# Kernel tuning notes

Measured on AMD Instinct MI355X. Metric: run time of the kernel, lower is better.

Reference implementation:

```python
import jax, jax.numpy as jnp
import numpy as np

BN_EPS = 1e-5

def _conv1x1(x, W, b):
    # x: [B,C,H,W], W: [O,C], b: [O]
    return jnp.einsum('bchw,oc->bohw', x, W) + b[None, :, None, None]

def setup_inputs() -> dict:
    key = jax.random.key(0)
    ks = jax.random.split(key, 9)
    B, C, H, W = 8, 256, 64, 64
    Ci = C // 2
    s_in = 0.05  # small init scale to keep softmax well-conditioned
    return {
        'x': jax.random.normal(ks[0], (B, C, H, W), jnp.float32),
        'theta_w': jax.random.normal(ks[1], (Ci, C), jnp.float32) * s_in,
        'theta_b': jnp.zeros((Ci,), jnp.float32),
        'phi_w': jax.random.normal(ks[2], (Ci, C), jnp.float32) * s_in,
        'phi_b': jnp.zeros((Ci,), jnp.float32),
        'g_w': jax.random.normal(ks[3], (Ci, C), jnp.float32) * s_in,
        'g_b': jnp.zeros((Ci,), jnp.float32),
        'out_w': jax.random.normal(ks[4], (C, Ci), jnp.float32) * s_in,
        'out_b': jnp.zeros((C,), jnp.float32),
        'gamma': jnp.ones((C,), jnp.float32),
        'beta': jnp.zeros((C,), jnp.float32),
    }

def reference(x, theta_w, theta_b, phi_w, phi_b, g_w, g_b, out_w, out_b, gamma, beta):
    B, C, H, W = x.shape
    Ci = C // 2
    N = H * W
    theta = _conv1x1(x, theta_w, theta_b).reshape(B, Ci, N)  # [B,Ci,N]
    phi = _conv1x1(x, phi_w, phi_b).reshape(B, Ci, N)        # [B,Ci,N]
    g = _conv1x1(x, g_w, g_b).reshape(B, Ci, N)              # [B,Ci,N]
    scale = 1.0 / jnp.sqrt(jnp.asarray(Ci, x.dtype))
    sim = jnp.einsum('bcn,bcm->bnm', theta, phi) * scale     # [B,N,N]
    attn = jax.nn.softmax(sim, axis=-1)
    y = jnp.einsum('bnm,bcm->bcn', attn, g).reshape(B, Ci, H, W)
    y = _conv1x1(y, out_w, out_b)                            # [B,C,H,W]
    # BatchNorm2d, training-mode statistics (biased variance), as in torch default
    mean = y.mean(axis=(0, 2, 3))
    var = y.var(axis=(0, 2, 3))
    y = (y - mean[None, :, None, None]) * jax.lax.rsqrt(var + BN_EPS)[None, :, None, None]
    y = y * gamma[None, :, None, None] + beta[None, :, None, None]
    return x + y
```

## Files before the change

kernel.cpp:

```cpp
#include <hip/hip_runtime.h>
#include <hip/hip_bf16.h>

typedef __bf16 bf16x8 __attribute__((ext_vector_type(8)));
typedef float f32x4 __attribute__((ext_vector_type(4)));
typedef float f32x16 __attribute__((ext_vector_type(16)));

#define B_ 8
#define C_ 256
#define CI 128
#define N_ 4096

__device__ __forceinline__ float exp2fast(float x) {
    return __builtin_amdgcn_exp2f(x);
}
__device__ __forceinline__ ushort f2bf(float f) {
    union { float f; unsigned u; } v; v.f = f;
    unsigned r = v.u + 0x7fffu + ((v.u >> 16) & 1u);
    return (ushort)(r >> 16);
}
__device__ __forceinline__ float bf2f(ushort u) {
    union { unsigned u; float f; } v; v.u = ((unsigned)u) << 16;
    return v.f;
}
__device__ __forceinline__ unsigned cvtpk(float lo, float hi) {
    unsigned r;
    asm("v_cvt_pk_bf16_f32 %0, %1, %2" : "=v"(r) : "v"(lo), "v"(hi));
    return r;
}
__device__ __forceinline__ void plswap(unsigned& a, unsigned& b) {
    asm volatile("v_permlane32_swap_b32 %0, %1" : "+v"(a), "+v"(b));
}
__device__ __forceinline__ void gld16(const void* src, void* dst) {
    __builtin_amdgcn_global_load_lds(
        (const __attribute__((address_space(1))) unsigned*)src,
        (__attribute__((address_space(3))) unsigned*)dst, 16, 0, 0);
}

__global__ void k_prep(const float* __restrict__ tw, const float* __restrict__ pw,
                       const float* __restrict__ gw, const float* __restrict__ ow,
                       ushort* __restrict__ wbf, ushort* __restrict__ owbf) {
    int idx = blockIdx.x * 256 + threadIdx.x;
    if (idx < 384 * 256) {
        int i = idx >> 8, c = idx & 255;
        float v = (i < 128) ? tw[i * 256 + c]
                : (i < 256) ? pw[(i - 128) * 256 + c]
                            : gw[(i - 256) * 256 + c];
        wbf[idx] = f2bf(v);
    }
    if (idx < 256 * 128) owbf[idx] = f2bf(ow[idx]);
}

__global__ __launch_bounds__(256) void k_transpose(const float* __restrict__ x,
                                                   ushort* __restrict__ xt) {
    __shared__ __align__(16) float tile[64][65];
    int b = blockIdx.z, c0 = blockIdx.y * 64, n0 = blockIdx.x * 64;
    int t = threadIdx.x;
    int cl = t >> 2, nc = (t & 3) * 16;
    const float* src = x + ((size_t)(b * 256 + c0 + cl)) * N_ + n0 + nc;
#pragma unroll
    for (int j = 0; j < 4; j++) {
        float4 v = *reinterpret_cast<const float4*>(src + 4 * j);
        tile[cl][nc + 4 * j + 0] = v.x;
        tile[cl][nc + 4 * j + 1] = v.y;
        tile[cl][nc + 4 * j + 2] = v.z;
        tile[cl][nc + 4 * j + 3] = v.w;
    }
    __syncthreads();
    int nl = t >> 2, cc = (t & 3) * 16;
    ushort* dst = xt + ((size_t)b * N_ + n0 + nl) * 256 + c0 + cc;
#pragma unroll
    for (int j = 0; j < 4; j++) {
        ushort4 o;
        o.x = f2bf(tile[cc + 4 * j + 0][nl]);
        o.y = f2bf(tile[cc + 4 * j + 1][nl]);
        o.z = f2bf(tile[cc + 4 * j + 2][nl]);
        o.w = f2bf(tile[cc + 4 * j + 3][nl]);
        *reinterpret_cast<ushort4*>(dst + 4 * j) = o;
    }
}

__global__ __launch_bounds__(256) void k_qkv(const ushort* __restrict__ wbf,
                                             const ushort* __restrict__ xt,
                                             const float* __restrict__ tb,
                                             const float* __restrict__ pb,
                                             const float* __restrict__ gb,
                                             ushort* __restrict__ qt,
                                             ushort* __restrict__ kt,
                                             ushort* __restrict__ gv) {
    __shared__ __align__(16) ushort lt[4][64][72];
    int nt = blockIdx.x, it = blockIdx.y, b = blockIdx.z;
    int tid = threadIdx.x, w = tid >> 6, l = tid & 63, lr = l & 15, lg = l >> 4;
    int i_off = it * 128 + (w >> 1) * 64;
    int n_off = nt * 128 + (w & 1) * 64;
    const ushort* xb = xt + (size_t)b * N_ * 256;

    f32x4 acc[4][4];
#pragma unroll
    for (int i = 0; i < 4; i++)
#pragma unroll
        for (int j = 0; j < 4; j++) acc[i][j] = (f32x4)0.0f;

#pragma unroll
    for (int kc = 0; kc < 8; kc++) {
        int ko = kc * 32 + lg * 8;
        bf16x8 a[4], bb[4];
#pragma unroll
        for (int fi = 0; fi < 4; fi++)
            a[fi] = *reinterpret_cast<const bf16x8*>(wbf + (size_t)(i_off + fi * 16 + lr) * 256 + ko);
#pragma unroll
        for (int fn = 0; fn < 4; fn++)
            bb[fn] = *reinterpret_cast<const bf16x8*>(xb + (size_t)(n_off + fn * 16 + lr) * 256 + ko);
#pragma unroll
        for (int fi = 0; fi < 4; fi++)
#pragma unroll
            for (int fn = 0; fn < 4; fn++)
                acc[fi][fn] = __builtin_amdgcn_mfma_f32_16x16x32_bf16(a[fi], bb[fn], acc[fi][fn], 0, 0, 0);
    }

    const float* bias = (it == 0) ? tb : (it == 1) ? pb : gb;
    const float mul = (it == 0) ? (0.08838834764831845f * 1.4426950408889634f) : 1.0f;
    if (it == 2) {
        ushort* g = gv + (size_t)b * CI * N_;
#pragma unroll
        for (int fi = 0; fi < 4; fi++)
#pragma unroll
            for (int reg = 0; reg < 4; reg++) {
                int cl = (w >> 1) * 64 + fi * 16 + lg * 4 + reg;
                float bv = bias[cl];
#pragma unroll
                for (int fn = 0; fn < 4; fn++)
                    g[(size_t)cl * N_ + n_off + fn * 16 + lr] = f2bf(acc[fi][fn][reg] + bv);
            }
    } else {
#pragma unroll
        for (int fi = 0; fi < 4; fi++)
#pragma unroll
            for (int reg = 0; reg < 4; reg++) {
                int il = fi * 16 + lg * 4 + reg;
                float bv = bias[(w >> 1) * 64 + il];
#pragma unroll
                for (int fn = 0; fn < 4; fn++)
                    lt[w][fn * 16 + lr][il] = f2bf((acc[fi][fn][reg] + bv) * mul);
            }
        __builtin_amdgcn_s_waitcnt(0);
        ushort* dst = ((it == 0) ? qt : kt) + (size_t)b * N_ * CI;
        ushort* drow = dst + (size_t)(n_off + l) * CI + (w >> 1) * 64;
#pragma unroll
        for (int cc = 0; cc < 8; cc++) {
            uint4 v = *reinterpret_cast<uint4*>(&lt[w][l][cc * 8]);
            *reinterpret_cast<uint4*>(drow + cc * 8) = v;
        }
    }
}

__global__ __launch_bounds__(256, 2) void k_attn(const ushort* __restrict__ qt,
                                                 const ushort* __restrict__ kt,
                                                 const ushort* __restrict__ gv,
                                                 ushort* __restrict__ yt) {
    __shared__ __align__(16) char smem[65536];
    int bid = blockIdx.x;
    int b = bid & 7, qb = bid >> 3;
    int tid = threadIdx.x, w = tid >> 6, l = tid & 63;
    int p = w >> 1, s = w & 1;
    int l31 = l & 31, lh = l >> 5;
    const ushort* qtb = qt + (size_t)b * N_ * CI;
    const ushort* ktb = kt + (size_t)b * N_ * CI;
    const ushort* gvb = gv + (size_t)b * CI * N_;
    char* kbuf = smem + p * 16384;
    char* vbuf = smem + 32768 + p * 16384;
    const int pbase = p * 2048;
    const int nq = qb * 64 + s * 32;
    const int q = nq + l31;
    const int swk = (l31 & 7) << 4;
    const int swv = (l31 & 3) << 4;

    bf16x8 qf[8];
#pragma unroll
    for (int kc = 0; kc < 8; kc++)
        qf[kc] = *reinterpret_cast<const bf16x8*>(qtb + (size_t)q * CI + kc * 16 + lh * 8);

    f32x16 acc[4];
#pragma unroll
    for (int fc = 0; fc < 4; fc++) acc[fc] = (f32x16)0.0f;
    float mrun = -1e30f, lrun = 0.f;

#define STAGE(t_, bi)                                                              \
    do {                                                                           \
        int m0_ = pbase + (t_) * 32;                                               \
        const char* ks_ = (const char*)(ktb + (size_t)m0_ * CI);                   \
        const char* vs_ = (const char*)gvb + (size_t)m0_ * 2;                      \
        char* kd_ = kbuf + (bi) * 8192;                                            \
        char* vd_ = vbuf + (bi) * 8192;                                            \
        _Pragma("unroll")                                                          \
        for (int i_ = 0; i_ < 4; ++i_) {                                           \
            int cc = i_ * 128 + s * 64 + l;                                        \
            int m_ = cc >> 4, hb = (cc & 15) << 4;                                 \
            gld16(ks_ + m_ * 256 + (hb ^ ((m_ & 7) << 4)), kd_ + cc * 16);         \
        }                                                                          \
        _Pragma("unroll")                                                          \
        for (int i_ = 0; i_ < 4; ++i_) {                                           \
            int cc = i_ * 128 + s * 64 + l;                                        \
            int c_ = cc >> 2, hb = (cc & 3) << 4;                                  \
            gld16(vs_ + (size_t)c_ * (N_ * 2) + (hb ^ ((c_ & 3) << 4)),            \
                  vd_ + cc * 16);                                                  \
        }                                                                          \
    } while (0)

    STAGE(0, 0);
    __syncthreads();

    for (int t = 0; t < 64; ++t) {
        int cur = t & 1;
        if (t < 63) STAGE(t + 1, cur ^ 1);
        const char* kbc = kbuf + cur * 8192;
        const char* vbc = vbuf + cur * 8192;

        f32x16 S = (f32x16)0.0f;
#pragma unroll
        for (int kc = 0; kc < 8; kc++) {
            bf16x8 kf = *reinterpret_cast<const bf16x8*>(
                kbc + l31 * 256 + ((kc * 32 + lh * 16) ^ swk));
            S = __builtin_amdgcn_mfma_f32_32x32x16_bf16(kf, qf[kc], S, 0, 0, 0);
        }

        float mx = S[0];
#pragma unroll
        for (int r = 1; r < 16; r++) mx = fmaxf(mx, S[r]);
        mx = fmaxf(mx, __shfl_xor(mx, 32));
        if (__any(mx > mrun + 8.f)) {
            float mn = fmaxf(mrun, mx);
            float corr = exp2fast(mrun - mn);
            mrun = mn;
            lrun *= corr;
#pragma unroll
            for (int fc = 0; fc < 4; fc++) acc[fc] *= corr;
        }
        float pv[16];
        float rs = 0.f;
#pragma unroll
        for (int r = 0; r < 16; r++) {
            pv[r] = exp2fast(S[r] - mrun);
            rs += pv[r];
        }
        rs += __shfl_xor(rs, 32);
        lrun += rs;

        unsigned u0 = cvtpk(pv[0], pv[1]),  u1 = cvtpk(pv[2], pv[3]);
        unsigned u2 = cvtpk(pv[4], pv[5]),  u3 = cvtpk(pv[6], pv[7]);
        unsigned u4 = cvtpk(pv[8], pv[9]),  u5 = cvtpk(pv[10], pv[11]);
        unsigned u6 = cvtpk(pv[12], pv[13]), u7 = cvtpk(pv[14], pv[15]);
        plswap(u0, u2);
        plswap(u1, u3);
        plswap(u4, u6);
        plswap(u5, u7);
        union { unsigned u[4]; bf16x8 v; } pb0, pb1;
        pb0.u[0] = u0; pb0.u[1] = u1; pb0.u[2] = u2; pb0.u[3] = u3;
        pb1.u[0] = u4; pb1.u[1] = u5; pb1.u[2] = u6; pb1.u[3] = u7;

#pragma unroll
        for (int mk = 0; mk < 2; mk++) {
            bf16x8 pf = mk ? pb1.v : pb0.v;
#pragma unroll
            for (int fc = 0; fc < 4; fc++) {
                bf16x8 vf = *reinterpret_cast<const bf16x8*>(
                    vbc + (fc * 32 + l31) * 64 + ((mk * 32 + lh * 16) ^ swv));
                acc[fc] = __builtin_amdgcn_mfma_f32_32x32x16_bf16(vf, pf, acc[fc], 0, 0, 0);
            }
        }
        __syncthreads();
    }
#undef STAGE

    float* accb = (float*)smem;
    float* mlb = (float*)(smem + 34816);
    if (p == 0) {
        float* ab = accb + s * (64 * 68) + l * 68;
#pragma unroll
        for (int fc = 0; fc < 4; fc++)
            *reinterpret_cast<f32x16*>(ab + fc * 16) = acc[fc];
        if (l < 32) {
            mlb[s * 32 + l] = mrun;
            mlb[64 + s * 32 + l] = lrun;
        }
    }
    __syncthreads();
    if (p == 1) {
        float m0 = mlb[s * 32 + l31], l0 = mlb[64 + s * 32 + l31];
        float mf = fmaxf(mrun, m0);
        float e1 = exp2fast(mrun - mf), e0 = exp2fast(m0 - mf);
        float inv = 1.f / (lrun * e1 + l0 * e0);
        e1 *= inv;
        e0 *= inv;
        const float* ab = accb + s * (64 * 68) + l * 68;
        ushort* yb = yt + (size_t)b * N_ * CI + (size_t)q * CI;
#pragma unroll
        for (int fc = 0; fc < 4; fc++) {
            f32x16 a0 = *reinterpret_cast<const f32x16*>(ab + fc * 16);
#pragma unroll
            for (int rg = 0; rg < 4; rg++) {
                ushort4 o;
                o.x = f2bf(acc[fc][rg * 4 + 0] * e1 + a0[rg * 4 + 0] * e0);
                o.y = f2bf(acc[fc][rg * 4 + 1] * e1 + a0[rg * 4 + 1] * e0);
                o.z = f2bf(acc[fc][rg * 4 + 2] * e1 + a0[rg * 4 + 2] * e0);
                o.w = f2bf(acc[fc][rg * 4 + 3] * e1 + a0[rg * 4 + 3] * e0);
                *reinterpret_cast<ushort4*>(yb + fc * 32 + rg * 8 + lh * 4) = o;
            }
        }
    }
}

__global__ __launch_bounds__(256) void k_outconv(const ushort* __restrict__ owbf,
                                                 const ushort* __restrict__ yt,
                                                 const float* __restrict__ ob,
                                                 ushort* __restrict__ pre,
                                                 float* __restrict__ part) {
    int nt = blockIdx.x, ot = blockIdx.y, b = blockIdx.z;
    int tid = threadIdx.x, w = tid >> 6, l = tid & 63, lr = l & 15, lg = l >> 4;
    int o_off = ot * 128 + (w >> 1) * 64;
    int n_off = nt * 128 + (w & 1) * 64;
    const ushort* yb = yt + (size_t)b * N_ * CI;

    f32x4 acc[4][4];
#pragma unroll
    for (int i = 0; i < 4; i++)
#pragma unroll
        for (int j = 0; j < 4; j++) acc[i][j] = (f32x4)0.0f;

#pragma unroll
    for (int kc = 0; kc < 4; kc++) {
        int ko = kc * 32 + lg * 8;
        bf16x8 a[4], bb[4];
#pragma unroll
        for (int fo = 0; fo < 4; fo++)
            a[fo] = *reinterpret_cast<const bf16x8*>(owbf + (size_t)(o_off + fo * 16 + lr) * CI + ko);
#pragma unroll
        for (int fn = 0; fn < 4; fn++)
            bb[fn] = *reinterpret_cast<const bf16x8*>(yb + (size_t)(n_off + fn * 16 + lr) * CI + ko);
#pragma unroll
        for (int fo = 0; fo < 4; fo++)
#pragma unroll
            for (int fn = 0; fn < 4; fn++)
                acc[fo][fn] = __builtin_amdgcn_mfma_f32_16x16x32_bf16(a[fo], bb[fn], acc[fo][fn], 0, 0, 0);
    }

    ushort* pb_ = pre + (size_t)b * C_ * N_;
#pragma unroll
    for (int fo = 0; fo < 4; fo++)
#pragma unroll
        for (int reg = 0; reg < 4; reg++) {
            int o = o_off + fo * 16 + lg * 4 + reg;
            float bv = ob[o];
            float s1 = 0.f, s2 = 0.f;
#pragma unroll
            for (int fn = 0; fn < 4; fn++) {
                float v = acc[fo][fn][reg] + bv;
                pb_[(size_t)o * N_ + n_off + fn * 16 + lr] = f2bf(v);
                s1 += v;
                s2 += v * v;
            }
#pragma unroll
            for (int d = 1; d < 16; d <<= 1) {
                s1 += __shfl_xor(s1, d);
                s2 += __shfl_xor(s2, d);
            }
            if (lr == 0) {
                int slot = (b * 32 + nt) * 2 + (w & 1);
                part[((size_t)o * 512 + slot) * 2 + 0] = s1;
                part[((size_t)o * 512 + slot) * 2 + 1] = s2;
            }
        }
}

__global__ void k_stats(const float* __restrict__ part, const float* __restrict__ gamma,
                        const float* __restrict__ beta, float* __restrict__ stats) {
    int o = blockIdx.x, t = threadIdx.x;
    __shared__ float r1[256], r2[256];
    float s1 = part[((size_t)o * 512 + t) * 2 + 0] + part[((size_t)o * 512 + t + 256) * 2 + 0];
    float s2 = part[((size_t)o * 512 + t) * 2 + 1] + part[((size_t)o * 512 + t + 256) * 2 + 1];
    r1[t] = s1; r2[t] = s2;
    __syncthreads();
    for (int s = 128; s > 0; s >>= 1) {
        if (t < s) { r1[t] += r1[t + s]; r2[t] += r2[t + s]; }
        __syncthreads();
    }
    if (t == 0) {
        float cnt = 1.f / (float)(B_ * N_);
        float mean = r1[0] * cnt;
        float var = r2[0] * cnt - mean * mean;
        float inv = rsqrtf(var + 1e-5f);
        float a = gamma[o] * inv;
        stats[o * 2 + 0] = a;
        stats[o * 2 + 1] = beta[o] - mean * a;
    }
}

__global__ void k_final(const float* __restrict__ x, const ushort* __restrict__ pre,
                        const float* __restrict__ stats, float* __restrict__ out) {
    int idx = blockIdx.x * 256 + threadIdx.x;
    int o = (idx >> 10) & 255;
    float a = stats[o * 2 + 0], c = stats[o * 2 + 1];
    float4 xv = reinterpret_cast<const float4*>(x)[idx];
    ushort4 pv = reinterpret_cast<const ushort4*>(pre)[idx];
    float4 ov;
    ov.x = xv.x + bf2f(pv.x) * a + c;
    ov.y = xv.y + bf2f(pv.y) * a + c;
    ov.z = xv.z + bf2f(pv.z) * a + c;
    ov.w = xv.w + bf2f(pv.w) * a + c;
    reinterpret_cast<float4*>(out)[idx] = ov;
}

extern "C" void kernel_launch(void* const* d_in, const int* in_sizes, int n_in,
                              void* d_out, int out_size, void* d_ws, size_t ws_size,
                              hipStream_t stream) {
    const float* x  = (const float*)d_in[0];
    const float* tw = (const float*)d_in[1];
    const float* tb = (const float*)d_in[2];
    const float* pw = (const float*)d_in[3];
    const float* pb = (const float*)d_in[4];
    const float* gw = (const float*)d_in[5];
    const float* gb = (const float*)d_in[6];
    const float* ow = (const float*)d_in[7];
    const float* ob = (const float*)d_in[8];
    const float* gamma = (const float*)d_in[9];
    const float* beta  = (const float*)d_in[10];

    char* ws = (char*)d_ws;
    const size_t WBF_OFF  = 0;
    const size_t OWBF_OFF = WBF_OFF + 196608;
    const size_t XT_OFF   = OWBF_OFF + 65536;
    const size_t QT_OFF   = XT_OFF + 16777216;
    const size_t KT_OFF   = QT_OFF + 8388608;
    const size_t GV_OFF   = KT_OFF + 8388608;
    const size_t YT_OFF   = GV_OFF + 8388608;
    const size_t PRE_OFF  = YT_OFF + 8388608;
    const size_t PART_OFF = PRE_OFF + 16777216;
    const size_t ST_OFF   = PART_OFF + 1048576;

    ushort* wbf  = (ushort*)(ws + WBF_OFF);
    ushort* owbf = (ushort*)(ws + OWBF_OFF);
    ushort* xt   = (ushort*)(ws + XT_OFF);
    ushort* qt   = (ushort*)(ws + QT_OFF);
    ushort* kt   = (ushort*)(ws + KT_OFF);
    ushort* gv   = (ushort*)(ws + GV_OFF);
    ushort* yt   = (ushort*)(ws + YT_OFF);
    ushort* pre  = (ushort*)(ws + PRE_OFF);
    float*  part = (float*)(ws + PART_OFF);
    float*  stats= (float*)(ws + ST_OFF);

    k_prep<<<384, 256, 0, stream>>>(tw, pw, gw, ow, wbf, owbf);
    k_transpose<<<dim3(64, 4, 8), 256, 0, stream>>>(x, xt);
    k_qkv<<<dim3(32, 3, 8), 256, 0, stream>>>(wbf, xt, tb, pb, gb, qt, kt, gv);
    k_attn<<<512, 256, 0, stream>>>(qt, kt, gv, yt);
    k_outconv<<<dim3(32, 2, 8), 256, 0, stream>>>(owbf, yt, ob, pre, part);
    k_stats<<<256, 256, 0, stream>>>(part, gamma, beta, stats);
    k_final<<<8192, 256, 0, stream>>>(x, pre, stats, (float*)d_out);
}
```

Baseline: 176.4 us.

## Relayout K/V shared tiles and overlap next-tile prefetch with compute

Changes the LDS layout of the K and V tiles so each thread's global-to-LDS copy uses a simple strided address and MFMA fragment reads become base-plus-constant offsets, replacing the XOR swizzle. Replaces __syncthreads with raw s_barrier plus an explicit vmcnt(8) wait, so the prefetch of the next tile stays in flight while the current tile is consumed. The loop now always issues a stage, including one past the end at t=63, which reads beyond the buffer range and is only drained by the final wait. This relies on the manual waitcnt being correct.

After: 206.6 us. 1.17x slower.

```diff
diff --git a/kernel.cpp b/kernel.cpp
--- a/kernel.cpp
+++ b/kernel.cpp
@@ -171,8 +171,9 @@
     const int pbase = p * 2048;
     const int nq = qb * 64 + s * 32;
     const int q = nq + l31;
-    const int swk = (l31 & 7) << 4;
-    const int swv = (l31 & 3) << 4;
+
+    const int krb = (l31 & 7) * 16 + lh * 128 + (l31 >> 3) * 2048;
+    const int vrb = (l31 & 7) * 16 + lh * 128 + (l31 >> 3) * 512;
 
     bf16x8 qf[8];
 #pragma unroll
@@ -188,38 +189,38 @@
     do {                                                                           \
         int m0_ = pbase + (t_) * 32;                                               \
         const char* ks_ = (const char*)(ktb + (size_t)m0_ * CI);                   \
-        const char* vs_ = (const char*)gvb + (size_t)m0_ * 2;                      \
-        char* kd_ = kbuf + (bi) * 8192;                                            \
-        char* vd_ = vbuf + (bi) * 8192;                                            \
+        const char* vs_ = (const char*)(gvb + (size_t)m0_);                        \
+        char* kd_ = kbuf + (bi) * 8192 + s * 1024;                                 \
+        char* vd_ = vbuf + (bi) * 8192 + s * 1024;                                 \
+        const char* ksl = ks_ + (l & 7) * 256 + (s * 8 + (l >> 3)) * 16;           \
+        const char* vsl = vs_ + ((size_t)((l & 7) + s * 16 + (l >> 5) * 8)) * 8192 \
+                              + ((l >> 3) & 3) * 16;                               \
         _Pragma("unroll")                                                          \
-        for (int i_ = 0; i_ < 4; ++i_) {                                           \
-            int cc = i_ * 128 + s * 64 + l;                                        \
-            int m_ = cc >> 4, hb = (cc & 15) << 4;                                 \
-            gld16(ks_ + m_ * 256 + (hb ^ ((m_ & 7) << 4)), kd_ + cc * 16);         \
-        }                                                                          \
+        for (int i_ = 0; i_ < 4; ++i_)                                             \
+            gld16(ksl + i_ * 2048, kd_ + i_ * 2048);                               \
         _Pragma("unroll")                                                          \
-        for (int i_ = 0; i_ < 4; ++i_) {                                           \
-            int cc = i_ * 128 + s * 64 + l;                                        \
-            int c_ = cc >> 2, hb = (cc & 3) << 4;                                  \
-            gld16(vs_ + (size_t)c_ * (N_ * 2) + (hb ^ ((c_ & 3) << 4)),            \
-                  vd_ + cc * 16);                                                  \
-        }                                                                          \
+        for (int i_ = 0; i_ < 4; ++i_)                                             \
+            gld16(vsl + (size_t)i_ * 262144, vd_ + i_ * 2048);                     \
     } while (0)
 
     STAGE(0, 0);
-    __syncthreads();
+    asm volatile("s_waitcnt vmcnt(0)" ::: "memory");
+    __builtin_amdgcn_s_barrier();
+    asm volatile("" ::: "memory");
 
     for (int t = 0; t < 64; ++t) {
         int cur = t & 1;
-        if (t < 63) STAGE(t + 1, cur ^ 1);
+        STAGE(t + 1, cur ^ 1);
+        asm volatile("s_waitcnt vmcnt(8)" ::: "memory");
+        __builtin_amdgcn_s_barrier();
+        asm volatile("" ::: "memory");
         const char* kbc = kbuf + cur * 8192;
         const char* vbc = vbuf + cur * 8192;
 
         f32x16 S = (f32x16)0.0f;
 #pragma unroll
         for (int kc = 0; kc < 8; kc++) {
-            bf16x8 kf = *reinterpret_cast<const bf16x8*>(
-                kbc + l31 * 256 + ((kc * 32 + lh * 16) ^ swk));
+            bf16x8 kf = *reinterpret_cast<const bf16x8*>(kbc + krb + kc * 256);
             S = __builtin_amdgcn_mfma_f32_32x32x16_bf16(kf, qf[kc], S, 0, 0, 0);
         }
 
@@ -262,14 +263,19 @@
             bf16x8 pf = mk ? pb1.v : pb0.v;
 #pragma unroll
             for (int fc = 0; fc < 4; fc++) {
-                bf16x8 vf = *reinterpret_cast<const bf16x8*>(
-                    vbc + (fc * 32 + l31) * 64 + ((mk * 32 + lh * 16) ^ swv));
+                bf16x8 vf = *reinterpret_cast<const bf16x8*>(vbc + vrb + mk * 256 + fc * 2048);
                 acc[fc] = __builtin_amdgcn_mfma_f32_32x32x16_bf16(vf, pf, acc[fc], 0, 0, 0);
             }
         }
-        __syncthreads();
+        asm volatile("" ::: "memory");
+        __builtin_amdgcn_s_barrier();
+        asm volatile("" ::: "memory");
     }
 #undef STAGE
+
+    asm volatile("s_waitcnt vmcnt(0)" ::: "memory");
+    __builtin_amdgcn_s_barrier();
+    asm volatile("" ::: "memory");
 
     float* accb = (float*)smem;
     float* mlb = (float*)(smem + 34816);
```
